# Optimization experiments

Hardware: AMD Instinct MI355X
Metric: run time of the kernel (lower is better)

## Reference

```python
import jax, jax.numpy as jnp
import numpy as np

B, C, H, W = 4, 256, 48, 48
HEADS, DH = 8, 32
INNER = HEADS * DH
HID = 128  # max(16, INNER//2)
SCALE = DH ** -0.5
EPS = 1e-6


def setup_inputs() -> dict:
    key = jax.random.key(0)
    ks = jax.random.split(key, 32)
    s = 0.02
    inp = {
        'x': jax.random.normal(ks[0], (B, C, H, W), jnp.float32),
        'rgb_input': jax.random.uniform(ks[1], (B, 3, H, W), jnp.float32),
        'wq': jax.random.normal(ks[2], (INNER, C), jnp.float32) * s,
        'bq': jnp.zeros((INNER,), jnp.float32),
        'wk': jax.random.normal(ks[3], (INNER, C), jnp.float32) * s,
        'bk': jnp.zeros((INNER,), jnp.float32),
        'wv': jax.random.normal(ks[4], (INNER, C), jnp.float32) * s,
        'bv': jnp.zeros((INNER,), jnp.float32),
        'wproj': jax.random.normal(ks[5], (C, INNER), jnp.float32) * s,
        'bproj': jnp.zeros((C,), jnp.float32),
        'c1_w': jax.random.normal(ks[6], (HID, 1, 3, 3), jnp.float32) * s,
        'c1_b': jnp.zeros((HID,), jnp.float32),
        'c2_w': jax.random.normal(ks[7], (HID, HID, 3, 3), jnp.float32) * s,
        'c2_b': jnp.zeros((HID,), jnp.float32),
        'gq_w': jax.random.normal(ks[8], (INNER, HID), jnp.float32) * s,
        'gq_b': jnp.ones((INNER,), jnp.float32),
        'bqf_w': jax.random.normal(ks[9], (INNER, HID), jnp.float32) * s,
        'bqf_b': jnp.zeros((INNER,), jnp.float32),
        'gk_w': jax.random.normal(ks[10], (INNER, HID), jnp.float32) * s,
        'gk_b': jnp.ones((INNER,), jnp.float32),
        'bkf_w': jax.random.normal(ks[11], (INNER, HID), jnp.float32) * s,
        'bkf_b': jnp.zeros((INNER,), jnp.float32),
        'gv_w': jax.random.normal(ks[12], (INNER, HID), jnp.float32) * s,
        'gv_b': jnp.ones((INNER,), jnp.float32),
        'bvf_w': jax.random.normal(ks[13], (INNER, HID), jnp.float32) * s,
        'bvf_b': jnp.zeros((INNER,), jnp.float32),
        'alpha': jnp.float32(0.1),
    }
    return inp


def _conv3(x, w, b):
    y = jax.lax.conv_general_dilated(x, w, (1, 1), 'SAME',
                                     dimension_numbers=('NCHW', 'OIHW', 'NCHW'))
    return y + b[None, :, None, None]


def _rgb_to_luma(rgb):
    y = 0.299 * rgb[:, 0:1] + 0.587 * rgb[:, 1:2] + 0.114 * rgb[:, 2:3]
    y_min = jnp.min(y, axis=(2, 3), keepdims=True)
    y_max = jnp.max(y, axis=(2, 3), keepdims=True)
    return (y - y_min) / (y_max - y_min + EPS)


def reference(x, rgb_input, wq, bq, wk, bk, wv, bv, wproj, bproj,
              c1_w, c1_b, c2_w, c2_b,
              gq_w, gq_b, bqf_w, bqf_b, gk_w, gk_b, bkf_w, bkf_b,
              gv_w, gv_b, bvf_w, bvf_b, alpha):
    Bx, Cx, Hx, Wx = x.shape
    N = Hx * Wx
    luma = _rgb_to_luma(rgb_input)  # [B,1,H,W]

    # LumaCond trunk + FiLM params (1x1 convs then global spatial mean)
    h = jax.nn.relu(_conv3(luma, c1_w, c1_b))
    h = jax.nn.relu(_conv3(h, c2_w, c2_b))
    hm = h.mean(axis=(2, 3))  # [B,HID] (mean commutes with 1x1 conv)

    def film_params(gw, gb, bw, bb):
        g = hm @ gw.T + gb  # [B, INNER]
        bta = hm @ bw.T + bb
        return (g.reshape(Bx, HEADS, DH, 1), bta.reshape(Bx, HEADS, DH, 1))

    gq, fbq = film_params(gq_w, gq_b, bqf_w, bqf_b)
    gk, fbk = film_params(gk_w, gk_b, bkf_w, bkf_b)
    gv, fbv = film_params(gv_w, gv_b, bvf_w, bvf_b)

    def proj_film(w, b, g, bta):
        t = jnp.einsum('bchw,oc->bohw', x, w) + b[None, :, None, None]
        t = t.reshape(Bx, HEADS, DH, N)
        return g * t + bta  # [B,heads,dh,N]

    q = proj_film(wq, bq, gq, fbq)
    k = proj_film(wk, bk, gk, fbk)
    v = proj_film(wv, bv, gv, fbv)

    logits = jnp.einsum('bhdn,bhdm->bhnm', q, k) * SCALE  # [B,heads,N,N]

    # luma bias: avg-pooled inverse luma, mean-centered per image
    invL = 1.0 - luma
    invL = jax.lax.reduce_window(invL, 0.0, jax.lax.add,
                                 (1, 1, 3, 3), (1, 1, 1, 1), 'SAME') / 9.0
    invL = invL.reshape(Bx, N)
    invL = invL - invL.mean(axis=-1, keepdims=True)
    logits = logits + alpha * invL[:, None, None, :]

    attn = jax.nn.softmax(logits, axis=-1)
    out = jnp.einsum('bhnm,bhdm->bhdn', attn, v)  # [B,heads,dh,N]
    out = out.reshape(Bx, INNER, Hx, Wx)
    return jnp.einsum('bchw,oc->bohw', out, wproj) + bproj[None, :, None, None]
```

## Files before the change

### kernel.cpp

```cpp
#include <hip/hip_runtime.h>


#define NSP 2304
#define WID 48

typedef __attribute__((ext_vector_type(4))) float  fvec4;
typedef __attribute__((ext_vector_type(2))) unsigned int uvec2;
typedef __attribute__((ext_vector_type(4))) unsigned int uvec4;
typedef __attribute__((ext_vector_type(8))) short  short8;
typedef __attribute__((ext_vector_type(4))) float  f32x4;

__device__ inline unsigned short f2bf(float f){
  unsigned int u = __builtin_bit_cast(unsigned int, f);
  u += 0x7fffu + ((u >> 16) & 1u);
  return (unsigned short)(u >> 16);
}
__device__ inline unsigned pack2bf(float a, float b){
#if __has_builtin(__builtin_amdgcn_cvt_pk_bf16_f32)
  typedef __attribute__((ext_vector_type(2))) __bf16 bf16x2;
  bf16x2 r = __builtin_amdgcn_cvt_pk_bf16_f32(a, b);
  return __builtin_bit_cast(unsigned, r);
#else
  return (unsigned)f2bf(a) | ((unsigned)f2bf(b) << 16);
#endif
}

__global__ void k0b_wcast(const float* __restrict__ c2w, const float* __restrict__ wq,
                          const float* __restrict__ wk, const float* __restrict__ wv_,
                          const float* __restrict__ wproj,
                          unsigned short* __restrict__ wtb,
                          unsigned short* __restrict__ wqkvb,
                          unsigned short* __restrict__ wprojb){
  int idx = blockIdx.x*256 + threadIdx.x;
  if (idx < 147456){
    int ic = idx & 127, rem = idx >> 7;
    int oc = rem & 127, tap = rem >> 7;
    wtb[idx] = f2bf(c2w[(oc*128 + ic)*9 + tap]);
  } else if (idx < 344064){
    int j = idx - 147456;
    int mat = j >> 16, oc_ = j & 65535;
    const float* src = (mat == 0) ? wq : (mat == 1) ? wk : wv_;
    wqkvb[j] = f2bf(src[oc_]);
  } else {
    int j = idx - 344064;
    wprojb[j] = f2bf(wproj[j]);
  }
}

__global__ __launch_bounds__(256) void k0xt(const float* __restrict__ x,
                                            unsigned short* __restrict__ xt){
  int nt = blockIdx.x, cc = blockIdx.y, b = blockIdx.z, t = threadIdx.x;
  __shared__ unsigned short tb[64*72];
  int cl0 = t >> 4;
  int nl0 = (t & 15) * 4;
  #pragma unroll
  for (int ps = 0; ps < 4; ++ps){
    int cl = cl0 + ps*16;
    fvec4 v = *(const fvec4*)(x + ((size_t)(b*256 + cc*64 + cl))*NSP + nt*64 + nl0);
    #pragma unroll
    for (int i = 0; i < 4; ++i) tb[(nl0+i)*72 + cl] = f2bf(v[i]);
  }
  __syncthreads();
  int nl = t >> 2, cg = (t & 3) * 16;
  uvec4 u0 = *(const uvec4*)&tb[nl*72 + cg];
  uvec4 u1 = *(const uvec4*)&tb[nl*72 + cg + 8];
  unsigned short* dst = xt + ((size_t)(b*NSP + nt*64 + nl))*256 + cc*64 + cg;
  *(uvec4*)dst = u0;
  *(uvec4*)(dst + 8) = u1;
}

__global__ __launch_bounds__(1024) void k1_luma(const float* __restrict__ rgb,
                        const float* __restrict__ alphaP,
                        float* __restrict__ luma_n, float* __restrict__ bias_a,
                        float* __restrict__ hm_sum, unsigned short* __restrict__ h1p){
  int b = blockIdx.x, t = threadIdx.x;
  __shared__ float ly[NSP];
  __shared__ float ll[NSP];
  __shared__ float red[1024];
  __shared__ float red2[1024];
  {
    const uvec4 z = {0u,0u,0u,0u};
    for (int j = t; j < 196*16; j += 1024){
      int cell = j >> 4, q = j & 15;
      int r, c;
      if (cell < 50)      { r = 0;           c = cell; }
      else if (cell < 100){ r = 49;          c = cell - 50; }
      else if (cell < 148){ r = cell - 99;   c = 0; }
      else                { r = cell - 147;  c = 49; }
      *(uvec4*)(h1p + ((size_t)(b*2500 + r*50 + c))*128 + q*8) = z;
    }
  }
  const float* rp = rgb + b*3*NSP;
  float lmin = 1e30f, lmax = -1e30f;
  for (int i = t; i < NSP; i += 1024){
    float y = 0.299f*rp[i] + 0.587f*rp[NSP+i] + 0.114f*rp[2*NSP+i];
    ly[i] = y; lmin = fminf(lmin, y); lmax = fmaxf(lmax, y);
  }
  red[t] = lmin; red2[t] = lmax;
  __syncthreads();
  for (int s = 512; s > 0; s >>= 1){
    if (t < s){ red[t] = fminf(red[t], red[t+s]); red2[t] = fmaxf(red2[t], red2[t+s]); }
    __syncthreads();
  }
  float mn = red[0], mx = red2[0];
  float inv = 1.0f / (mx - mn + 1e-6f);
  for (int i = t; i < NSP; i += 1024){
    float v = (ly[i] - mn) * inv;
    ll[i] = v;
    luma_n[b*NSP + i] = v;
  }
  if (t < 128) hm_sum[b*128 + t] = 0.f;
  __syncthreads();
  float pr[3]; float psum = 0.f;
  #pragma unroll
  for (int ii = 0; ii < 3; ++ii){
    int n = t + 1024*ii;
    pr[ii] = 0.f;
    if (n < NSP){
      int row = n / WID, col = n - row*WID;
      float s = 0.f;
      #pragma unroll
      for (int dy = -1; dy <= 1; ++dy)
        #pragma unroll
        for (int dx = -1; dx <= 1; ++dx){
          int r2 = row+dy, c2 = col+dx;
          if (r2 >= 0 && r2 < WID && c2 >= 0 && c2 < WID) s += 1.0f - ll[r2*WID + c2];
        }
      pr[ii] = s * (1.f/9.f);
      psum += pr[ii];
    }
  }
  __syncthreads();
  red[t] = psum;
  __syncthreads();
  for (int s = 512; s > 0; s >>= 1){
    if (t < s) red[t] += red[t+s];
    __syncthreads();
  }
  float mean = red[0] * (1.f/(float)NSP);
  float alpha = alphaP[0] * 1.4426950408889634f;
  #pragma unroll
  for (int ii = 0; ii < 3; ++ii){
    int n = t + 1024*ii;
    if (n < NSP) bias_a[b*NSP + n] = alpha * (pr[ii] - mean);
  }
}

__global__ void k2_conv1(const float* __restrict__ luma_n, const float* __restrict__ c1w,
                         const float* __restrict__ c1b, unsigned short* __restrict__ h1p){
  int nt = blockIdx.x, ocg = blockIdx.y, b = blockIdx.z, t = threadIdx.x;
  __shared__ float wsm[32*9];
  __shared__ float bsm[32];
  for (int i = t; i < 288; i += 256) wsm[i] = c1w[ocg*288 + i];
  if (t < 32) bsm[t] = c1b[ocg*32 + t];
  __syncthreads();
  int n = nt*256 + t;
  int row = n / WID, col = n - row*WID;
  const float* lp = luma_n + b*NSP;
  float lv[9];
  int k = 0;
  #pragma unroll
  for (int dy = -1; dy <= 1; ++dy)
    #pragma unroll
    for (int dx = -1; dx <= 1; ++dx, ++k){
      int r2 = row+dy, c2 = col+dx;
      lv[k] = (r2 >= 0 && r2 < WID && c2 >= 0 && c2 < WID) ? lp[r2*WID + c2] : 0.f;
    }
  unsigned int packed[16];
  #pragma unroll
  for (int oc2 = 0; oc2 < 16; ++oc2){
    float a0 = bsm[oc2*2], a1 = bsm[oc2*2+1];
    #pragma unroll
    for (int q = 0; q < 9; ++q){
      a0 += wsm[(oc2*2)*9 + q] * lv[q];
      a1 += wsm[(oc2*2+1)*9 + q] * lv[q];
    }
    packed[oc2] = pack2bf(fmaxf(a0, 0.f), fmaxf(a1, 0.f));
  }
  unsigned short* dst = h1p + ((size_t)(b*2500 + (row+1)*50 + (col+1)))*128 + ocg*32;
  #pragma unroll
  for (int q4 = 0; q4 < 4; ++q4)
    *(uvec4*)(dst + q4*8) = *(uvec4*)&packed[q4*4];
}

__global__ __launch_bounds__(256) void k3_conv2(const unsigned short* __restrict__ h1p,
    const unsigned short* __restrict__ wtb, const float* __restrict__ c2b,
    float* __restrict__ hm_sum){
  int row = blockIdx.x, mh = blockIdx.y, b = blockIdx.z;
  int t = threadIdx.x, wv = t >> 6, lane = t & 63;
  int lq = lane >> 4, lc = lane & 15;
  int ocb = mh*64 + wv*16;
  const f32x4 z4 = {0.f, 0.f, 0.f, 0.f};
  f32x4 C[3] = {z4, z4, z4};
  const unsigned short* hbase = h1p + (size_t)b*2500*128;
  #pragma unroll
  for (int tap = 0; tap < 9; ++tap){
    int dy = tap/3 - 1, dx = tap%3 - 1;
    const unsigned short* wrow = wtb + (tap*128 + ocb + lc)*128 + lq*8;
    const unsigned short* hrow = hbase + ((row+dy+1)*50 + (dx+1) + lc)*128 + lq*8;
    #pragma unroll
    for (int kc = 0; kc < 4; ++kc){
      short8 aW = *(const short8*)(wrow + kc*32);
      #pragma unroll
      for (int ntp = 0; ntp < 3; ++ntp){
        short8 bH = *(const short8*)(hrow + ntp*16*128 + kc*32);
        C[ntp] = __builtin_amdgcn_mfma_f32_16x16x32_bf16(aW, bH, C[ntp], 0, 0, 0);
      }
    }
  }
  float s[4];
  #pragma unroll
  for (int r = 0; r < 4; ++r){
    float bias = c2b[ocb + lq*4 + r];
    float v = 0.f;
    #pragma unroll
    for (int ntp = 0; ntp < 3; ++ntp) v += fmaxf(C[ntp][r] + bias, 0.f);
    v += __shfl_xor(v, 1, 64);
    v += __shfl_xor(v, 2, 64);
    v += __shfl_xor(v, 4, 64);
    v += __shfl_xor(v, 8, 64);
    s[r] = v;
  }
  if (lc == 0){
    #pragma unroll
    for (int r = 0; r < 4; ++r)
      atomicAdd(&hm_sum[b*128 + ocb + lq*4 + r], s[r]);
  }
}

__global__ void k4_film(const float* __restrict__ hm_sum,
  const float* w0, const float* b0, const float* w1, const float* b1,
  const float* w2, const float* b2, const float* w3, const float* b3,
  const float* w4, const float* b4, const float* w5, const float* b5,
  float* __restrict__ film){
  __shared__ float hs[128];
  int bb = blockIdx.x & 3, m6 = blockIdx.x >> 2, t = threadIdx.x;
  if (t < 128) hs[t] = hm_sum[bb*128 + t] * (1.f/(float)NSP);
  __syncthreads();
  const float* wm[6] = {w0,w1,w2,w3,w4,w5};
  const float* bm[6] = {b0,b1,b2,b3,b4,b5};
  const float* w = wm[m6];
  int o = t;
  float a = bm[m6][o];
  for (int h2 = 0; h2 < 128; ++h2) a += hs[h2] * w[o*128 + h2];
  film[blockIdx.x*256 + t] = a;
}

__global__ __launch_bounds__(256) void k5_qkv(const unsigned short* __restrict__ xt,
    const unsigned short* __restrict__ wqkvb,
    const float* __restrict__ bq, const float* __restrict__ bk, const float* __restrict__ bv,
    const float* __restrict__ film,
    unsigned short* __restrict__ q_t, unsigned short* __restrict__ k_t,
    unsigned short* __restrict__ v_b){
  int nt = blockIdx.x, ot = blockIdx.y, b = blockIdx.z;
  int t = threadIdx.x, wv = t >> 6, lane = t & 63;
  int lq = lane >> 4, lc = lane & 15;
  int p = ot >> 1;
  int omb = (ot & 1)*128 + wv*32;
  const f32x4 z4 = {0.f, 0.f, 0.f, 0.f};
  f32x4 acc[2][4];
  #pragma unroll
  for (int oh = 0; oh < 2; ++oh)
    #pragma unroll
    for (int nq = 0; nq < 4; ++nq) acc[oh][nq] = z4;

  const unsigned short* wbp = wqkvb + p*65536 + (omb + lc)*256 + lq*8;
  const unsigned short* xbp = xt + ((size_t)(b*NSP + nt*64 + lc))*256 + lq*8;

  short8 aW0[2], aW1[2], bX0[4], bX1[4];
  auto loadW = [&](short8 (&W)[2], int kc){
    #pragma unroll
    for (int oh = 0; oh < 2; ++oh) W[oh] = *(const short8*)(wbp + oh*16*256 + kc*32);
  };
  auto loadX = [&](short8 (&X)[4], int kc){
    #pragma unroll
    for (int nq = 0; nq < 4; ++nq) X[nq] = *(const short8*)(xbp + (size_t)nq*16*256 + kc*32);
  };
  auto mm = [&](short8 (&W)[2], short8 (&X)[4]){
    #pragma unroll
    for (int oh = 0; oh < 2; ++oh)
      #pragma unroll
      for (int nq = 0; nq < 4; ++nq)
        acc[oh][nq] = __builtin_amdgcn_mfma_f32_16x16x32_bf16(W[oh], X[nq], acc[oh][nq], 0, 0, 0);
  };
  loadW(aW0, 0); loadX(bX0, 0);
  for (int kc2 = 0; kc2 < 4; ++kc2){
    loadW(aW1, kc2*2+1); loadX(bX1, kc2*2+1);
    mm(aW0, bX0);
    int kn = (kc2*2+2) & 7;
    loadW(aW0, kn); loadX(bX0, kn);
    mm(aW1, bX1);
  }

  const float* bvec = (p == 0) ? bq : (p == 1) ? bk : bv;
  int hq = omb >> 5;
  unsigned short* qk = (p == 0) ? q_t : k_t;
  #pragma unroll
  for (int oh = 0; oh < 2; ++oh){
    fvec4 g4 = *(const fvec4*)(film + (2*p*4 + b)*256 + omb + oh*16 + lq*4);
    fvec4 t4 = *(const fvec4*)(film + ((2*p+1)*4 + b)*256 + omb + oh*16 + lq*4);
    fvec4 z4b = *(const fvec4*)(bvec + omb + oh*16 + lq*4);
    #pragma unroll
    for (int nq = 0; nq < 4; ++nq){
      int n = nt*64 + nq*16 + lc;
      float v0 = g4[0]*(acc[oh][nq][0] + z4b[0]) + t4[0];
      float v1 = g4[1]*(acc[oh][nq][1] + z4b[1]) + t4[1];
      float v2 = g4[2]*(acc[oh][nq][2] + z4b[2]) + t4[2];
      float v3 = g4[3]*(acc[oh][nq][3] + z4b[3]) + t4[3];
      if (p == 0){
        const float sc = 0.17677669529663687f * 1.4426950408889634f;
        v0 *= sc; v1 *= sc; v2 *= sc; v3 *= sc;
      }
      if (p < 2){
        uvec2 u;
        u.x = pack2bf(v0, v1);
        u.y = pack2bf(v2, v3);
        *(uvec2*)(qk + ((size_t)((b*8 + hq)*NSP + n))*32 + oh*16 + lq*4) = u;
      } else {
        int om = omb + oh*16 + lq*4;
        v_b[((size_t)(b*256 + om + 0))*NSP + n] = f2bf(v0);
        v_b[((size_t)(b*256 + om + 1))*NSP + n] = f2bf(v1);
        v_b[((size_t)(b*256 + om + 2))*NSP + n] = f2bf(v2);
        v_b[((size_t)(b*256 + om + 3))*NSP + n] = f2bf(v3);
      }
    }
  }
}

__global__ __launch_bounds__(256, 4) void k6_attn(const unsigned short* __restrict__ q_t,
    const unsigned short* __restrict__ k_t, const unsigned short* __restrict__ v_b,
    const float* __restrict__ bias_a,
    unsigned short* __restrict__ o0, unsigned short* __restrict__ o1,
    float* __restrict__ l0, float* __restrict__ l1){
  int bx = blockIdx.x, h = blockIdx.y, b = blockIdx.z;
  int qblk = bx >> 1, s = bx & 1;
  unsigned short* op = s ? o1 : o0;
  float* lp = s ? l1 : l0;
  int t = threadIdx.x, wv = t >> 6, lane = t & 63;
  int lq = lane >> 4, lc = lane & 15;
  int bh = b*8 + h;
  int nb0 = qblk*128 + wv*32;
  const f32x4 z4 = {0.f, 0.f, 0.f, 0.f};
  int ms = s*1152;

  __shared__ float ps[4][1024];
  float* myps = ps[wv];
  int sxm = ((lc&7)<<2) | (((lc>>3)&1)<<1);
  int wbase = lc*32;

  const unsigned short* kfr = k_t + ((size_t)(bh*NSP + ms + lc))*32 + lq*8;
  const unsigned short* vfr = v_b + ((size_t)(b*256 + h*32 + lc))*NSP + ms + lq*8;
  const float* brow = bias_a + b*NSP + ms;

  short8 aQ[2];
  #pragma unroll
  for (int qf = 0; qf < 2; ++qf)
    aQ[qf] = *(const short8*)(q_t + ((size_t)(bh*NSP + nb0 + qf*16 + lc))*32 + lq*8);

  fvec4 c0r[4];
  #pragma unroll
  for (int g = 0; g < 4; ++g) c0r[g] = *(const fvec4*)(brow + g*16 + lq*4);

  const uvec4 onesu = {0x3F803F80u, 0x3F803F80u, 0x3F803F80u, 0x3F803F80u};
  const short8 aOnes = __builtin_bit_cast(short8, onesu);

  f32x4 O[2][2]; f32x4 Ol[2];
  #pragma unroll
  for (int qf = 0; qf < 2; ++qf){
    Ol[qf] = z4; O[qf][0] = z4; O[qf][1] = z4;
  }

  short8 aKA[4], aKB[4];
  #pragma unroll
  for (int g = 0; g < 4; ++g)
    aKA[g] = *(const short8*)(kfr + (size_t)g*512);

  auto body = [&](short8 (&AK)[4], int it){
    int m0 = it*64;
    short8 aV[2][2];
    #pragma unroll
    for (int dhg = 0; dhg < 2; ++dhg)
      #pragma unroll
      for (int mh = 0; mh < 2; ++mh)
        aV[dhg][mh] = *(const short8*)(vfr + (size_t)dhg*16*NSP + m0 + mh*32);
    #pragma unroll
    for (int qf = 0; qf < 2; ++qf){
      #pragma unroll
      for (int g = 0; g < 4; ++g){
        f32x4 S = __builtin_amdgcn_mfma_f32_16x16x32_bf16(AK[g], aQ[qf], c0r[g], 0, 0, 0);
        uvec2 w2;
        w2.x = pack2bf(__builtin_amdgcn_exp2f(S[0]), __builtin_amdgcn_exp2f(S[1]));
        w2.y = pack2bf(__builtin_amdgcn_exp2f(S[2]), __builtin_amdgcn_exp2f(S[3]));
        *(uvec2*)&myps[qf*512 + wbase + ((g*8 + lq*2) ^ sxm)] = w2;
      }
    }
    if (it < 17){
      #pragma unroll
      for (int g = 0; g < 4; ++g)
        c0r[g] = *(const fvec4*)(brow + (it+1)*64 + g*16 + lq*4);
    }
    __builtin_amdgcn_s_setprio(1);
    #pragma unroll
    for (int qf = 0; qf < 2; ++qf){
      #pragma unroll
      for (int mh = 0; mh < 2; ++mh){
        int d0 = (mh*16 + lq*4) ^ sxm;
        uvec2 lo = *(const uvec2*)&myps[qf*512 + wbase + d0];
        uvec2 hi = *(const uvec2*)&myps[qf*512 + wbase + (d0 ^ 2)];
        uvec4 up; up.x = lo.x; up.y = lo.y; up.z = hi.x; up.w = hi.y;
        short8 bP = __builtin_bit_cast(short8, up);
        Ol[qf] = __builtin_amdgcn_mfma_f32_16x16x32_bf16(aOnes, bP, Ol[qf], 0, 0, 0);
        #pragma unroll
        for (int dhg = 0; dhg < 2; ++dhg)
          O[qf][dhg] = __builtin_amdgcn_mfma_f32_16x16x32_bf16(aV[dhg][mh], bP, O[qf][dhg], 0, 0, 0);
      }
    }
    __builtin_amdgcn_s_setprio(0);
  };

  for (int it2 = 0; it2 < 9; ++it2){
    int it0 = it2*2;
    #pragma unroll
    for (int g = 0; g < 4; ++g)
      aKB[g] = *(const short8*)(kfr + (size_t)(it0+1)*2048 + (size_t)g*512);
    body(aKA, it0);
    #pragma unroll
    for (int g = 0; g < 4; ++g)
      aKA[g] = *(const short8*)(kfr + (size_t)(it0+2)*2048 + (size_t)g*512);
    body(aKB, it0+1);
  }

  #pragma unroll
  for (int qf = 0; qf < 2; ++qf){
    int nidx = nb0 + qf*16 + lc;
    if (lq == 0) lp[b*NSP + nidx] = Ol[qf][0];
    #pragma unroll
    for (int dh = 0; dh < 2; ++dh){
      uvec2 u;
      u.x = pack2bf(O[qf][dh][0], O[qf][dh][1]);
      u.y = pack2bf(O[qf][dh][2], O[qf][dh][3]);
      *(uvec2*)(op + ((size_t)(b*NSP + nidx))*256 + h*32 + dh*16 + lq*4) = u;
    }
  }
}

__global__ __launch_bounds__(256) void k7_proj(const unsigned short* __restrict__ a0,
    const unsigned short* __restrict__ a1, const float* __restrict__ l0p,
    const float* __restrict__ l1p, const unsigned short* __restrict__ wprojb,
    const float* __restrict__ bproj, float* __restrict__ out){
  int nt = blockIdx.x, ct = blockIdx.y, b = blockIdx.z;
  int t = threadIdx.x, wv = t >> 6, lane = t & 63;
  int lq = lane >> 4, lc = lane & 15;
  __shared__ float rls[32];
  if (t < 32) rls[t] = 1.0f / (l0p[b*NSP + nt*32 + t] + l1p[b*NSP + nt*32 + t]);
  __syncthreads();
  int cb = ct*128 + wv*32;
  const f32x4 z4 = {0.f, 0.f, 0.f, 0.f};
  f32x4 acc[2][2];
  #pragma unroll
  for (int ch = 0; ch < 2; ++ch)
    #pragma unroll
    for (int nq = 0; nq < 2; ++nq) acc[ch][nq] = z4;

  const unsigned short* wpp = wprojb + (cb + lc)*256 + lq*8;
  const unsigned short* a0p = a0 + ((size_t)(b*NSP + nt*32 + lc))*256 + lq*8;
  const unsigned short* a1p = a1 + ((size_t)(b*NSP + nt*32 + lc))*256 + lq*8;

  short8 W0[2], W1[2], p00[2], p01[2], p10[2], p11[2];
  auto loadS = [&](short8 (&W)[2], short8 (&B0)[2], short8 (&B1)[2], int kc){
    #pragma unroll
    for (int ch = 0; ch < 2; ++ch) W[ch] = *(const short8*)(wpp + ch*16*256 + kc*32);
    #pragma unroll
    for (int nq = 0; nq < 2; ++nq){
      B0[nq] = *(const short8*)(a0p + (size_t)nq*16*256 + kc*32);
      B1[nq] = *(const short8*)(a1p + (size_t)nq*16*256 + kc*32);
    }
  };
  auto mmS = [&](short8 (&W)[2], short8 (&B0)[2], short8 (&B1)[2]){
    #pragma unroll
    for (int ch = 0; ch < 2; ++ch)
      #pragma unroll
      for (int nq = 0; nq < 2; ++nq){
        acc[ch][nq] = __builtin_amdgcn_mfma_f32_16x16x32_bf16(W[ch], B0[nq], acc[ch][nq], 0, 0, 0);
        acc[ch][nq] = __builtin_amdgcn_mfma_f32_16x16x32_bf16(W[ch], B1[nq], acc[ch][nq], 0, 0, 0);
      }
  };
  loadS(W0, p00, p10, 0);
  for (int kc2 = 0; kc2 < 4; ++kc2){
    loadS(W1, p01, p11, kc2*2+1);
    mmS(W0, p00, p10);
    int kn = (kc2*2+2) & 7;
    loadS(W0, p00, p10, kn);
    mmS(W1, p01, p11);
  }

  #pragma unroll
  for (int ch = 0; ch < 2; ++ch){
    #pragma unroll
    for (int nq = 0; nq < 2; ++nq){
      int n = nt*32 + nq*16 + lc;
      float rl = rls[nq*16 + lc];
      #pragma unroll
      for (int r = 0; r < 4; ++r){
        int c = cb + ch*16 + lq*4 + r;
        out[((size_t)(b*256 + c))*NSP + n] = acc[ch][nq][r]*rl + bproj[c];
      }
    }
  }
}

extern "C" void kernel_launch(void* const* d_in, const int* in_sizes, int n_in,
                              void* d_out, int out_size, void* d_ws, size_t ws_size,
                              hipStream_t stream) {
  const float* x     = (const float*)d_in[0];
  const float* rgb   = (const float*)d_in[1];
  const float* wq    = (const float*)d_in[2];
  const float* bq    = (const float*)d_in[3];
  const float* wk    = (const float*)d_in[4];
  const float* bk    = (const float*)d_in[5];
  const float* wv    = (const float*)d_in[6];
  const float* bv    = (const float*)d_in[7];
  const float* wproj = (const float*)d_in[8];
  const float* bproj = (const float*)d_in[9];
  const float* c1w   = (const float*)d_in[10];
  const float* c1b   = (const float*)d_in[11];
  const float* c2w   = (const float*)d_in[12];
  const float* c2b   = (const float*)d_in[13];
  const float* gq_w  = (const float*)d_in[14];
  const float* gq_b  = (const float*)d_in[15];
  const float* bqf_w = (const float*)d_in[16];
  const float* bqf_b = (const float*)d_in[17];
  const float* gk_w  = (const float*)d_in[18];
  const float* gk_b  = (const float*)d_in[19];
  const float* bkf_w = (const float*)d_in[20];
  const float* bkf_b = (const float*)d_in[21];
  const float* gv_w  = (const float*)d_in[22];
  const float* gv_b  = (const float*)d_in[23];
  const float* bvf_w = (const float*)d_in[24];
  const float* bvf_b = (const float*)d_in[25];
  const float* alphaP= (const float*)d_in[26];

  char* w = (char*)d_ws;
  float* luma_n = (float*)w;            w += 4*NSP*4;
  float* bias_a = (float*)w;            w += 4*NSP*4;
  float* hm_sum = (float*)w;            w += 512*4;
  float* film   = (float*)w;            w += 6*4*256*4;
  unsigned short* h1p = (unsigned short*)w; w += 4*2500*128*2;
  unsigned short* wtb = (unsigned short*)w; w += 9*128*128*2;
  unsigned short* wqkvb = (unsigned short*)w; w += 3*256*256*2;
  unsigned short* wprojb = (unsigned short*)w; w += 256*256*2;
  unsigned short* xt  = (unsigned short*)w; w += (size_t)4*NSP*256*2;
  unsigned short* q_t = (unsigned short*)w; w += (size_t)4*8*NSP*32*2;
  unsigned short* k_t = (unsigned short*)w; w += (size_t)4*8*NSP*32*2;
  unsigned short* v_b = (unsigned short*)w; w += (size_t)4*256*NSP*2;
  unsigned short* o_part0 = (unsigned short*)w; w += (size_t)4*NSP*256*2;
  unsigned short* o_part1 = (unsigned short*)w; w += (size_t)4*NSP*256*2;
  float* l_part0 = (float*)w;           w += 4*NSP*4;
  float* l_part1 = (float*)w;           w += 4*NSP*4;

  k0b_wcast<<<1600, 256, 0, stream>>>(c2w, wq, wk, wv, wproj, wtb, wqkvb, wprojb);
  k0xt    <<<dim3(36,4,4), 256, 0, stream>>>(x, xt);
  k1_luma <<<4, 1024, 0, stream>>>(rgb, alphaP, luma_n, bias_a, hm_sum, h1p);
  k2_conv1<<<dim3(9,4,4), 256, 0, stream>>>(luma_n, c1w, c1b, h1p);
  k3_conv2<<<dim3(48,2,4), 256, 0, stream>>>(h1p, wtb, c2b, hm_sum);
  k4_film <<<24, 256, 0, stream>>>(hm_sum, gq_w, gq_b, bqf_w, bqf_b,
                                   gk_w, gk_b, bkf_w, bkf_b,
                                   gv_w, gv_b, bvf_w, bvf_b, film);
  k5_qkv  <<<dim3(36,6,4), 256, 0, stream>>>(xt, wqkvb, bq, bk, bv, film,
                                             q_t, k_t, v_b);
  k6_attn <<<dim3(36,8,4), 256, 0, stream>>>(q_t, k_t, v_b, bias_a,
                                             o_part0, o_part1, l_part0, l_part1);
  k7_proj <<<dim3(72,2,4), 256, 0, stream>>>(o_part0, o_part1, l_part0, l_part1,
                                             wprojb, bproj, (float*)d_out);
}
```

Baseline: 304.8 us.

## Stage K/V tiles in double-buffered LDS and software-pipeline the P·V step

The attention kernel now has all 256 threads cooperatively load each 64-key K and V tile once into swizzled, double-buffered shared memory. Previously each of the four waves fetched the same K/V fragments from global memory on its own. The P·V MFMA stage is also shifted one iteration behind the score/exp stage, so the previous tile's probability products overlap the current tile's scores. This cuts redundant global traffic but adds a __syncthreads per iteration, extra LDS use that may lower occupancy, and an epilogue to drain the last tile.

```diff
diff --git a/kernel.cpp b/kernel.cpp
--- a/kernel.cpp
+++ b/kernel.cpp
@@ -343,13 +343,22 @@
   const f32x4 z4 = {0.f, 0.f, 0.f, 0.f};
   int ms = s*1152;
 
+  __shared__ unsigned short Kb[2][64*32];
+  __shared__ unsigned short Vb[2][32*64];
   __shared__ float ps[4][1024];
   float* myps = ps[wv];
   int sxm = ((lc&7)<<2) | (((lc>>3)&1)<<1);
   int wbase = lc*32;
 
-  const unsigned short* kfr = k_t + ((size_t)(bh*NSP + ms + lc))*32 + lq*8;
-  const unsigned short* vfr = v_b + ((size_t)(b*256 + h*32 + lc))*NSP + ms + lq*8;
+  const unsigned short* kg = k_t + ((size_t)(bh*NSP + ms + (t>>2)))*32 + (t&3)*8;
+  const unsigned short* vg = v_b + ((size_t)(b*256 + h*32 + (t>>3)))*NSP + ms + (t&7)*8;
+  int krow = t >> 2;
+  unsigned short* kw = &Kb[0][krow*32 + (((t&3) ^ ((krow>>1)&3))*8)];
+  int vrow = t >> 3;
+  unsigned short* vw = &Vb[0][vrow*64 + (((t&7) ^ (vrow&7))*8)];
+
+  int kcol = (lq ^ ((lc>>1)&3))*8;
+
   const float* brow = bias_a + b*NSP + ms;
 
   short8 aQ[2];
@@ -370,65 +379,81 @@
     Ol[qf] = z4; O[qf][0] = z4; O[qf][1] = z4;
   }
 
-  short8 aKA[4], aKB[4];
-  #pragma unroll
-  for (int g = 0; g < 4; ++g)
-    aKA[g] = *(const short8*)(kfr + (size_t)g*512);
-
-  auto body = [&](short8 (&AK)[4], int it){
-    int m0 = it*64;
-    short8 aV[2][2];
-    #pragma unroll
-    for (int dhg = 0; dhg < 2; ++dhg)
-      #pragma unroll
-      for (int mh = 0; mh < 2; ++mh)
-        aV[dhg][mh] = *(const short8*)(vfr + (size_t)dhg*16*NSP + m0 + mh*32);
-    #pragma unroll
-    for (int qf = 0; qf < 2; ++qf){
-      #pragma unroll
-      for (int g = 0; g < 4; ++g){
-        f32x4 S = __builtin_amdgcn_mfma_f32_16x16x32_bf16(AK[g], aQ[qf], c0r[g], 0, 0, 0);
-        uvec2 w2;
-        w2.x = pack2bf(__builtin_amdgcn_exp2f(S[0]), __builtin_amdgcn_exp2f(S[1]));
-        w2.y = pack2bf(__builtin_amdgcn_exp2f(S[2]), __builtin_amdgcn_exp2f(S[3]));
-        *(uvec2*)&myps[qf*512 + wbase + ((g*8 + lq*2) ^ sxm)] = w2;
-      }
-    }
-    if (it < 17){
-      #pragma unroll
-      for (int g = 0; g < 4; ++g)
-        c0r[g] = *(const fvec4*)(brow + (it+1)*64 + g*16 + lq*4);
-    }
-    __builtin_amdgcn_s_setprio(1);
-    #pragma unroll
-    for (int qf = 0; qf < 2; ++qf){
+  short8 aK[4], aV[2][2], bP[2][2];
+
+  auto readP = [&](){
+    #pragma unroll
+    for (int qf = 0; qf < 2; ++qf)
       #pragma unroll
       for (int mh = 0; mh < 2; ++mh){
         int d0 = (mh*16 + lq*4) ^ sxm;
         uvec2 lo = *(const uvec2*)&myps[qf*512 + wbase + d0];
         uvec2 hi = *(const uvec2*)&myps[qf*512 + wbase + (d0 ^ 2)];
         uvec4 up; up.x = lo.x; up.y = lo.y; up.z = hi.x; up.w = hi.y;
-        short8 bP = __builtin_bit_cast(short8, up);
-        Ol[qf] = __builtin_amdgcn_mfma_f32_16x16x32_bf16(aOnes, bP, Ol[qf], 0, 0, 0);
+        bP[qf][mh] = __builtin_bit_cast(short8, up);
+      }
+  };
+  auto sphase = [&](){
+    #pragma unroll
+    for (int qf = 0; qf < 2; ++qf){
+      #pragma unroll
+      for (int g = 0; g < 4; ++g){
+        f32x4 S = __builtin_amdgcn_mfma_f32_16x16x32_bf16(aK[g], aQ[qf], c0r[g], 0, 0, 0);
+        uvec2 w2;
+        w2.x = pack2bf(__builtin_amdgcn_exp2f(S[0]), __builtin_amdgcn_exp2f(S[1]));
+        w2.y = pack2bf(__builtin_amdgcn_exp2f(S[2]), __builtin_amdgcn_exp2f(S[3]));
+        *(uvec2*)&myps[qf*512 + wbase + ((g*8 + lq*2) ^ sxm)] = w2;
+      }
+    }
+  };
+  auto pv = [&](){
+    __builtin_amdgcn_s_setprio(1);
+    #pragma unroll
+    for (int qf = 0; qf < 2; ++qf){
+      #pragma unroll
+      for (int mh = 0; mh < 2; ++mh){
+        Ol[qf] = __builtin_amdgcn_mfma_f32_16x16x32_bf16(aOnes, bP[qf][mh], Ol[qf], 0, 0, 0);
         #pragma unroll
         for (int dhg = 0; dhg < 2; ++dhg)
-          O[qf][dhg] = __builtin_amdgcn_mfma_f32_16x16x32_bf16(aV[dhg][mh], bP, O[qf][dhg], 0, 0, 0);
+          O[qf][dhg] = __builtin_amdgcn_mfma_f32_16x16x32_bf16(aV[dhg][mh], bP[qf][mh], O[qf][dhg], 0, 0, 0);
       }
     }
     __builtin_amdgcn_s_setprio(0);
   };
 
-  for (int it2 = 0; it2 < 9; ++it2){
-    int it0 = it2*2;
+  uvec4 gKr = *(const uvec4*)kg;
+  uvec4 gVr = *(const uvec4*)vg;
+
+  for (int it = 0; it < 18; ++it){
+    int buf = it & 1;
+    *(uvec4*)(kw + buf*2048) = gKr;
+    *(uvec4*)(vw + buf*2048) = gVr;
+    __syncthreads();
+    if (it < 17){
+      gKr = *(const uvec4*)(kg + (size_t)(it+1)*2048);
+      gVr = *(const uvec4*)(vg + (it+1)*64);
+    }
+    const unsigned short* kb = Kb[buf];
     #pragma unroll
     for (int g = 0; g < 4; ++g)
-      aKB[g] = *(const short8*)(kfr + (size_t)(it0+1)*2048 + (size_t)g*512);
-    body(aKA, it0);
-    #pragma unroll
-    for (int g = 0; g < 4; ++g)
-      aKA[g] = *(const short8*)(kfr + (size_t)(it0+2)*2048 + (size_t)g*512);
-    body(aKB, it0+1);
-  }
+      aK[g] = *(const short8*)(kb + (g*16 + lc)*32 + kcol);
+    if (it > 0) readP();
+    sphase();
+    if (it < 17){
+      #pragma unroll
+      for (int g = 0; g < 4; ++g)
+        c0r[g] = *(const fvec4*)(brow + (it+1)*64 + g*16 + lq*4);
+    }
+    if (it > 0) pv();
+    const unsigned short* vb = Vb[buf];
+    #pragma unroll
+    for (int dhg = 0; dhg < 2; ++dhg)
+      #pragma unroll
+      for (int mh = 0; mh < 2; ++mh)
+        aV[dhg][mh] = *(const short8*)(vb + (dhg*16 + lc)*64 + (((mh*4 + lq) ^ (lc&7))*8));
+  }
+  readP();
+  pv();
 
   #pragma unroll
   for (int qf = 0; qf < 2; ++qf){
```

Result: faster. 278.0 us (-8.8%).
